# Performance work log

Measured on AMD Instinct MI355X. Metric: run time of the kernel, lower is better.

## Reference

```python
import jax, jax.numpy as jnp
import numpy as np

EMBED_DIM = 768
NUM_HEADS = 12
HEAD_DIM = EMBED_DIM // NUM_HEADS  # 64
NUM_LEVELS = 2
Q_INDEX = (0, 6, 12)  # head-axis split per level
K_INDEX = (0, 6, 12)
V_INDEX = (0, 6, 12)


def setup_inputs() -> dict:
    key = jax.random.key(0)
    ks = jax.random.split(key, 12)
    std = 0.02
    d = {
        'inp0': jax.random.normal(ks[0], (8, 2048, 768), jnp.float32),
        'inp1': jax.random.normal(ks[1], (8, 1024, 1536), jnp.float32),
        'attn_mask': jax.random.normal(ks[2], (8, HEAD_DIM), jnp.float32),
        'Wq0': jax.random.normal(ks[3], (768, 768), jnp.float32) * std,
        'bq0': jnp.zeros((768,), jnp.float32),
        'Wk0': jax.random.normal(ks[4], (768, 768), jnp.float32) * std,
        'bk0': jnp.zeros((768,), jnp.float32),
        'Wv0': jax.random.normal(ks[5], (768, 768), jnp.float32) * std,
        'bv0': jnp.zeros((768,), jnp.float32),
        'Wq1': jax.random.normal(ks[6], (1536, 768), jnp.float32) * std,
        'bq1': jnp.zeros((768,), jnp.float32),
        'Wk1': jax.random.normal(ks[7], (1536, 768), jnp.float32) * std,
        'bk1': jnp.zeros((768,), jnp.float32),
        'Wv1': jax.random.normal(ks[8], (1536, 768), jnp.float32) * std,
        'bv1': jnp.zeros((768,), jnp.float32),
        'Wo': jax.random.normal(ks[9], (2 * 768, 768), jnp.float32) * std,
        'bo': jnp.zeros((768,), jnp.float32),
    }
    return d


def _split_heads(x):
    b, n, _ = x.shape
    return x.reshape(b, n, NUM_HEADS, HEAD_DIM).transpose(0, 2, 1, 3)  # b h n d


def _level_attention(level, inp, Wq, bq, Wk, bk, Wv, bv, attn_mask):
    q = _split_heads(inp @ Wq + bq)[:, Q_INDEX[level]:Q_INDEX[level + 1]]
    k = _split_heads(inp @ Wk + bk)[:, K_INDEX[level]:K_INDEX[level + 1]]
    v = _split_heads(inp @ Wv + bv)[:, V_INDEX[level]:V_INDEX[level + 1]]
    q = q * (HEAD_DIM ** -0.5)
    q = q + attn_mask[:, None, None, :]  # broadcast mask over heads & positions
    scores = jnp.einsum('bhnd,bhmd->bhnm', q, k)
    attn = jax.nn.softmax(scores, axis=-1)
    return jnp.einsum('bhnm,bhmd->bhnd', attn, v)  # b h n d


def reference(inp0, inp1, attn_mask, Wq0, bq0, Wk0, bk0, Wv0, bv0,
              Wq1, bq1, Wk1, bk1, Wv1, bv1, Wo, bo):
    levels = [
        (inp0, Wq0, bq0, Wk0, bk0, Wv0, bv0),
        (inp1, Wq1, bq1, Wk1, bk1, Wv1, bv1),
    ]
    outputs = [_level_attention(l, *args, attn_mask) for l, args in enumerate(levels)]
    n_max = max(o.shape[2] for o in outputs)
    merged, masks = [], []
    for o in outputs:
        b, h, n, dd = o.shape
        x = o.transpose(0, 2, 1, 3).reshape(b, n, h * dd)  # b n (h d)
        x = jnp.pad(x, ((0, 0), (0, n_max - n), (0, EMBED_DIM - h * dd)))
        merged.append(x)
        masks.append(jnp.pad(jnp.ones((n,), jnp.float32), (0, n_max - n)))
    x = jnp.concatenate(merged, axis=-1)  # [b, n_max, NUM_LEVELS*EMBED_DIM]
    output_mask = jnp.stack(masks)  # [NUM_LEVELS, n_max]
    output = x @ Wo + bo
    return (output, output_mask)
```

## Files before the change

### kernel.cpp

```cpp
#include <hip/hip_runtime.h>
#include <cmath>

typedef __bf16 bf16x8 __attribute__((ext_vector_type(8)));
typedef float floatx4 __attribute__((ext_vector_type(4)));

typedef __attribute__((address_space(1))) const void* as1_cvp;
typedef __attribute__((address_space(3))) void* as3_vp;

__device__ __forceinline__ void stage16(const void* g, void* l) {
    __builtin_amdgcn_global_load_lds((as1_cvp)g, (as3_vp)l, 16, 0, 0);
}

__global__ void prep_all(
    const float* __restrict__ inp0, const float* __restrict__ inp1,
    const float* __restrict__ Wq0, const float* __restrict__ Wk0, const float* __restrict__ Wv0,
    const float* __restrict__ Wq1, const float* __restrict__ Wk1, const float* __restrict__ Wv1,
    const float* __restrict__ Wo,
    __bf16* __restrict__ Ab0, __bf16* __restrict__ Ab1,
    __bf16* __restrict__ WT0, __bf16* __restrict__ WT1, __bf16* __restrict__ WoT)
{
    __shared__ __bf16 tile[64][72];
    const int bx = blockIdx.x;
    const int tid = threadIdx.x;

    if (bx < 12288) {
        const float* in  = (bx < 6144) ? inp0 : inp1;
        __bf16*      out = (bx < 6144) ? Ab0  : Ab1;
        int t = (bx < 6144 ? bx : bx - 6144) * 256 + tid;
        floatx4 f0 = *(const floatx4*)&in[(size_t)t * 8];
        floatx4 f1 = *(const floatx4*)&in[(size_t)t * 8 + 4];
        bf16x8 o;
#pragma unroll
        for (int j = 0; j < 4; j++) { o[j] = (__bf16)f0[j]; o[4 + j] = (__bf16)f1[j]; }
        *(bf16x8*)&out[(size_t)t * 8] = o;
        return;
    }

    int lane = tid & 63, tr = tid >> 6;

    if (bx < 12936) {
        int seg1 = (bx >= 12504);
        int idx = seg1 ? bx - 12504 : bx - 12288;
        int nkb = seg1 ? 24 : 12;
        int Kd  = seg1 ? 1536 : 768;
        int off = seg1 ? 384 : 0;
        int k0 = (idx % nkb) * 64, c0 = (idx / nkb) * 64;
        int proj = c0 / 384;
        const float* src = seg1 ? ((proj == 0) ? Wq1 : (proj == 1) ? Wk1 : Wv1)
                                : ((proj == 0) ? Wq0 : (proj == 1) ? Wk0 : Wv0);
        __bf16* WT = seg1 ? WT1 : WT0;
        int col = off + (c0 % 384) + lane;
#pragma unroll
        for (int i = 0; i < 16; i++) {
            int r = i * 4 + tr;
            tile[lane][r] = (__bf16)src[(size_t)(k0 + r) * 768 + col];
        }
        __syncthreads();
#pragma unroll
        for (int i = 0; i < 16; i++) {
            int cl = i * 4 + tr;
            WT[(size_t)(c0 + cl) * Kd + k0 + lane] = tile[cl][lane];
        }
        return;
    }

    {
        int idx = bx - 12936;
        int k0 = (idx % 12) * 64, c0 = (idx / 12) * 64;
        int col = c0 + lane;
#pragma unroll
        for (int i = 0; i < 16; i++) {
            int k = k0 + i * 4 + tr;
            int srow = k + (k >= 384 ? 384 : 0);
            tile[lane][i * 4 + tr] = (__bf16)Wo[(size_t)srow * 768 + col];
        }
        __syncthreads();
#pragma unroll
        for (int i = 0; i < 16; i++) {
            int cl = i * 4 + tr;
            WoT[(size_t)(c0 + cl) * 768 + k0 + lane] = tile[cl][lane];
        }
        return;
    }
}

__global__ __launch_bounds__(256, 2) void qkv_all(
    const __bf16* __restrict__ Ab0, const __bf16* __restrict__ Ab1,
    const __bf16* __restrict__ WT0, const __bf16* __restrict__ WT1,
    const float* __restrict__ bq0, const float* __restrict__ bk0, const float* __restrict__ bv0,
    const float* __restrict__ bq1, const float* __restrict__ bk1, const float* __restrict__ bv1,
    const float* __restrict__ mask,
    __bf16* __restrict__ Q0, __bf16* __restrict__ K0, __bf16* __restrict__ V0T,
    __bf16* __restrict__ Q1, __bf16* __restrict__ K1, __bf16* __restrict__ V1T)
{
    __shared__ __bf16 As[128 * 64];
    __shared__ __bf16 Bs[128 * 64];
    const int bx = blockIdx.x;
    const int seg = (bx >= 1152);
    const int idx = seg ? bx - 1152 : bx;
    const int Kd  = seg ? 1536 : 768;
    const int Nl  = seg ? 1024 : 2048;
    const int nlsh = seg ? 10 : 11;
    const int off = seg ? 384 : 0;
    const __bf16* A  = seg ? Ab1 : Ab0;
    const __bf16* BT = seg ? WT1 : WT0;
    const float* bq = seg ? bq1 : bq0;
    const float* bk = seg ? bk1 : bk0;
    const float* bv = seg ? bv1 : bv0;
    __bf16* Qo  = seg ? Q1 : Q0;
    __bf16* Ko  = seg ? K1 : K0;
    __bf16* VTo = seg ? V1T : V0T;

    const int tid = threadIdx.x;
    const int lane = tid & 63;
    const int wave = tid >> 6;
    const int lr = lane & 15, lg = lane >> 4;
    const int col0 = (idx % 9) * 128, row0 = (idx / 9) * 128;
    const int qr = (wave >> 1) * 64, qc = (wave & 1) * 64;
    floatx4 acc[4][4] = {};

    for (int k0 = 0; k0 < Kd; k0 += 64) {
        const __bf16* ga = A + (size_t)(row0 + wave * 32 + (lane >> 3)) * Kd + k0 + (lane & 7) * 8;
        const __bf16* gb = BT + (size_t)(col0 + wave * 32 + (lane >> 3)) * Kd + k0 + (lane & 7) * 8;
#pragma unroll
        for (int i = 0; i < 4; i++) {
            stage16(ga + (size_t)i * 8 * Kd, &As[(wave * 32 + i * 8) * 64]);
            stage16(gb + (size_t)i * 8 * Kd, &Bs[(wave * 32 + i * 8) * 64]);
        }
        __syncthreads();
#pragma unroll
        for (int ch = 0; ch < 2; ch++) {
            bf16x8 af[4], bfr[4];
#pragma unroll
            for (int mt = 0; mt < 4; mt++)
                af[mt] = *(const bf16x8*)&As[(qr + mt * 16 + lr) * 64 + ch * 32 + lg * 8];
#pragma unroll
            for (int nt = 0; nt < 4; nt++)
                bfr[nt] = *(const bf16x8*)&Bs[(qc + nt * 16 + lr) * 64 + ch * 32 + lg * 8];
#pragma unroll
            for (int mt = 0; mt < 4; mt++)
#pragma unroll
                for (int nt = 0; nt < 4; nt++)
                    acc[mt][nt] = __builtin_amdgcn_mfma_f32_16x16x32_bf16(af[mt], bfr[nt], acc[mt][nt], 0, 0, 0);
        }
        __syncthreads();
    }

    const float S_Q = 0.125f * 1.44269504088896f;
    const float S_M = 1.44269504088896f;
#pragma unroll
    for (int nt = 0; nt < 4; nt++) {
        int C = col0 + qc + nt * 16 + lr;
        int proj = C / 384;
        int rem = C - proj * 384;
        int h = rem >> 6, d = C & 63;
        float bias = (proj == 0) ? bq[off + rem]
                   : (proj == 1) ? bk[off + rem]
                                 : bv[off + rem];
#pragma unroll
        for (int mt = 0; mt < 4; mt++) {
#pragma unroll
            for (int r = 0; r < 4; r++) {
                int R = row0 + qr + mt * 16 + lg * 4 + r;
                int b = R >> nlsh;
                int n = R & (Nl - 1);
                size_t hb = (size_t)(b * 6 + h);
                float v = acc[mt][nt][r] + bias;
                if (proj == 0) {
                    v = fmaf(v, S_Q, S_M * mask[(b << 6) + d]);
                    Qo[(hb * Nl + n) * 64 + d] = (__bf16)v;
                } else if (proj == 1) {
                    Ko[(hb * Nl + n) * 64 + d] = (__bf16)v;
                } else {
                    VTo[(hb * 64 + d) * (size_t)Nl + n] = (__bf16)v;
                }
            }
        }
    }
}

__global__ __launch_bounds__(256, 4) void attn_all(
    const __bf16* __restrict__ Q0, const __bf16* __restrict__ K0, const __bf16* __restrict__ V0T,
    const __bf16* __restrict__ Q1, const __bf16* __restrict__ K1, const __bf16* __restrict__ V1T,
    __bf16* __restrict__ X, float* __restrict__ om)
{
    __shared__ __bf16 Ks[64 * 72];
    __shared__ __bf16 Vs[64 * 72];
    __shared__ __bf16 Ps[4][32 * 72];
    const int bx = blockIdx.x;
    const int tid = threadIdx.x;

    if (bx >= 1152) {
        int t = (bx - 1152) * 256 + tid;
        int r = t / 48;
        int c = (t - r * 48) * 8;
        int b = r >> 10, n = 1024 + (r & 1023);
        floatx4 z = {0.f, 0.f, 0.f, 0.f};
        *(floatx4*)&X[(size_t)(b * 2048 + n) * 768 + 384 + c] = z;
        if (t < 4096)
            om[t] = (t < 2048) ? 1.0f : (((t - 2048) < 1024) ? 1.0f : 0.0f);
        return;
    }

    const int seg = (bx >= 768);
    const int idx = seg ? bx - 768 : bx;
    const int Nl = seg ? 1024 : 2048;
    const int qb = seg ? (idx & 7) : (idx & 15);
    const int rest = seg ? (idx >> 3) : (idx >> 4);
    const int h = rest % 6, b = rest / 6;
    const int xoff = seg ? 384 : 0;
    const __bf16* Q  = seg ? Q1 : Q0;
    const __bf16* K  = seg ? K1 : K0;
    const __bf16* VT = seg ? V1T : V0T;

    const int wave = tid >> 6, lane = tid & 63;
    const int lr = lane & 15, lg = lane >> 4;
    const size_t head = (size_t)(b * 6 + h) * Nl * 64;
    const int q0 = qb * 128 + wave * 16;

    bf16x8 qf[2][2];
#pragma unroll
    for (int s = 0; s < 2; s++)
#pragma unroll
        for (int ch = 0; ch < 2; ch++)
            qf[s][ch] = *(const bf16x8*)&Q[head + (size_t)(q0 + s * 64 + lr) * 64 + ch * 32 + lg * 8];

    bf16x8 onesv;
#pragma unroll
    for (int j = 0; j < 8; j++) onesv[j] = (__bf16)1.0f;

    const int rr = tid >> 2, cc = (tid & 3) * 16;
    const __bf16* Kg = K + head;
    const __bf16* Vg = VT + head;

    bf16x8 kr0, kr1, vr0, vr1;
    {
        size_t kb = (size_t)rr * 64 + cc;
        kr0 = *(const bf16x8*)&Kg[kb];
        kr1 = *(const bf16x8*)&Kg[kb + 8];
        size_t vb = (size_t)rr * Nl + cc;
        vr0 = *(const bf16x8*)&Vg[vb];
        vr1 = *(const bf16x8*)&Vg[vb + 8];
    }

    floatx4 o_acc[2][4] = {};
    floatx4 l_acc[2] = {};

    for (int n0 = 0; n0 < Nl; n0 += 64) {
        __syncthreads();
        *(bf16x8*)&Ks[rr * 72 + cc]     = kr0;
        *(bf16x8*)&Ks[rr * 72 + cc + 8] = kr1;
        *(bf16x8*)&Vs[rr * 72 + cc]     = vr0;
        *(bf16x8*)&Vs[rr * 72 + cc + 8] = vr1;
        __syncthreads();

        if (n0 + 64 < Nl) {
            size_t kb = (size_t)(n0 + 64 + rr) * 64 + cc;
            kr0 = *(const bf16x8*)&Kg[kb];
            kr1 = *(const bf16x8*)&Kg[kb + 8];
            size_t vb = (size_t)rr * Nl + n0 + 64 + cc;
            vr0 = *(const bf16x8*)&Vg[vb];
            vr1 = *(const bf16x8*)&Vg[vb + 8];
        }

        floatx4 sv[2][4] = {};
#pragma unroll
        for (int ch = 0; ch < 2; ch++) {
#pragma unroll
            for (int nt = 0; nt < 4; nt++) {
                bf16x8 kb8 = *(const bf16x8*)&Ks[(nt * 16 + lr) * 72 + ch * 32 + lg * 8];
                sv[0][nt] = __builtin_amdgcn_mfma_f32_16x16x32_bf16(qf[0][ch], kb8, sv[0][nt], 0, 0, 0);
                sv[1][nt] = __builtin_amdgcn_mfma_f32_16x16x32_bf16(qf[1][ch], kb8, sv[1][nt], 0, 0, 0);
            }
        }

#pragma unroll
        for (int s = 0; s < 2; s++)
#pragma unroll
            for (int nt = 0; nt < 4; nt++)
#pragma unroll
                for (int r = 0; r < 4; r++) {
                    float p = __builtin_amdgcn_exp2f(sv[s][nt][r]);
                    Ps[wave][(s * 16 + lg * 4 + r) * 72 + nt * 16 + lr] = (__bf16)p;
                }
        asm volatile("s_waitcnt lgkmcnt(0)" ::: "memory");

#pragma unroll
        for (int ch = 0; ch < 2; ch++) {
            bf16x8 pa0 = *(const bf16x8*)&Ps[wave][lr * 72 + ch * 32 + lg * 8];
            bf16x8 pa1 = *(const bf16x8*)&Ps[wave][(16 + lr) * 72 + ch * 32 + lg * 8];
#pragma unroll
            for (int dt = 0; dt < 4; dt++) {
                bf16x8 vb8 = *(const bf16x8*)&Vs[(dt * 16 + lr) * 72 + ch * 32 + lg * 8];
                o_acc[0][dt] = __builtin_amdgcn_mfma_f32_16x16x32_bf16(pa0, vb8, o_acc[0][dt], 0, 0, 0);
                o_acc[1][dt] = __builtin_amdgcn_mfma_f32_16x16x32_bf16(pa1, vb8, o_acc[1][dt], 0, 0, 0);
            }
            l_acc[0] = __builtin_amdgcn_mfma_f32_16x16x32_bf16(pa0, onesv, l_acc[0], 0, 0, 0);
            l_acc[1] = __builtin_amdgcn_mfma_f32_16x16x32_bf16(pa1, onesv, l_acc[1], 0, 0, 0);
        }
    }

#pragma unroll
    for (int s = 0; s < 2; s++)
#pragma unroll
        for (int dt = 0; dt < 4; dt++)
#pragma unroll
            for (int r = 0; r < 4; r++) {
                int n = q0 + s * 64 + lg * 4 + r;
                float o = o_acc[s][dt][r] / l_acc[s][r];
                X[(size_t)(b * 2048 + n) * 768 + xoff + h * 64 + dt * 16 + lr] = (__bf16)o;
            }
}

__global__ __launch_bounds__(256, 2) void out_gemm(
    const __bf16* __restrict__ A, const __bf16* __restrict__ BT,
    const float* __restrict__ bo, float* __restrict__ out)
{
    __shared__ __bf16 As[128 * 64];
    __shared__ __bf16 Bs[128 * 64];
    const int tid = threadIdx.x;
    const int lane = tid & 63;
    const int wave = tid >> 6;
    const int lr = lane & 15, lg = lane >> 4;
    const int col0 = blockIdx.x * 128, row0 = blockIdx.y * 128;
    const int qr = (wave >> 1) * 64, qc = (wave & 1) * 64;
    const int Kd = 768;
    floatx4 acc[4][4] = {};

    for (int k0 = 0; k0 < Kd; k0 += 64) {
        const __bf16* ga = A + (size_t)(row0 + wave * 32 + (lane >> 3)) * Kd + k0 + (lane & 7) * 8;
        const __bf16* gb = BT + (size_t)(col0 + wave * 32 + (lane >> 3)) * Kd + k0 + (lane & 7) * 8;
#pragma unroll
        for (int i = 0; i < 4; i++) {
            stage16(ga + (size_t)i * 8 * Kd, &As[(wave * 32 + i * 8) * 64]);
            stage16(gb + (size_t)i * 8 * Kd, &Bs[(wave * 32 + i * 8) * 64]);
        }
        __syncthreads();
#pragma unroll
        for (int ch = 0; ch < 2; ch++) {
            bf16x8 af[4], bfr[4];
#pragma unroll
            for (int mt = 0; mt < 4; mt++)
                af[mt] = *(const bf16x8*)&As[(qr + mt * 16 + lr) * 64 + ch * 32 + lg * 8];
#pragma unroll
            for (int nt = 0; nt < 4; nt++)
                bfr[nt] = *(const bf16x8*)&Bs[(qc + nt * 16 + lr) * 64 + ch * 32 + lg * 8];
#pragma unroll
            for (int mt = 0; mt < 4; mt++)
#pragma unroll
                for (int nt = 0; nt < 4; nt++)
                    acc[mt][nt] = __builtin_amdgcn_mfma_f32_16x16x32_bf16(af[mt], bfr[nt], acc[mt][nt], 0, 0, 0);
        }
        __syncthreads();
    }

#pragma unroll
    for (int nt = 0; nt < 4; nt++) {
        int C = col0 + qc + nt * 16 + lr;
        float bias = bo[C];
#pragma unroll
        for (int mt = 0; mt < 4; mt++) {
#pragma unroll
            for (int r = 0; r < 4; r++) {
                int R = row0 + qr + mt * 16 + lg * 4 + r;
                out[(size_t)R * 768 + C] = acc[mt][nt][r] + bias;
            }
        }
    }
}

extern "C" void kernel_launch(void* const* d_in, const int* in_sizes, int n_in,
                              void* d_out, int out_size, void* d_ws, size_t ws_size,
                              hipStream_t stream)
{
    const float* inp0  = (const float*)d_in[0];
    const float* inp1  = (const float*)d_in[1];
    const float* amask = (const float*)d_in[2];
    const float* Wq0 = (const float*)d_in[3];
    const float* bq0 = (const float*)d_in[4];
    const float* Wk0 = (const float*)d_in[5];
    const float* bk0 = (const float*)d_in[6];
    const float* Wv0 = (const float*)d_in[7];
    const float* bv0 = (const float*)d_in[8];
    const float* Wq1 = (const float*)d_in[9];
    const float* bq1 = (const float*)d_in[10];
    const float* Wk1 = (const float*)d_in[11];
    const float* bk1 = (const float*)d_in[12];
    const float* Wv1 = (const float*)d_in[13];
    const float* bv1 = (const float*)d_in[14];
    const float* Wo  = (const float*)d_in[15];
    const float* bo  = (const float*)d_in[16];

    char* ws = (char*)d_ws;
    __bf16* WT0 = (__bf16*)(ws + 0);
    __bf16* WT1 = (__bf16*)(ws + 1769472);
    __bf16* WoT = (__bf16*)(ws + 5308416);
    __bf16* Ab0 = (__bf16*)(ws + 6488064);
    __bf16* X   = Ab0;
    __bf16* Ab1 = (__bf16*)(ws + 31653888);
    __bf16* Q0  = (__bf16*)(ws + 56819712);
    __bf16* K0  = (__bf16*)(ws + 69402624);
    __bf16* V0T = (__bf16*)(ws + 81985536);
    __bf16* Q1  = (__bf16*)(ws + 94568448);
    __bf16* K1  = (__bf16*)(ws + 100859904);
    __bf16* V1T = (__bf16*)(ws + 107151360);
    float* outp = (float*)d_out;

    hipLaunchKernelGGL(prep_all, dim3(13080), dim3(256), 0, stream,
                       inp0, inp1, Wq0, Wk0, Wv0, Wq1, Wk1, Wv1, Wo,
                       Ab0, Ab1, WT0, WT1, WoT);
    hipLaunchKernelGGL(qkv_all, dim3(1728), dim3(256), 0, stream,
                       Ab0, Ab1, WT0, WT1,
                       bq0, bk0, bv0, bq1, bk1, bv1, amask,
                       Q0, K0, V0T, Q1, K1, V1T);
    hipLaunchKernelGGL(attn_all, dim3(2688), dim3(256), 0, stream,
                       Q0, K0, V0T, Q1, K1, V1T, X, outp + 12582912);
    hipLaunchKernelGGL(out_gemm, dim3(6, 128), dim3(256), 0, stream,
                       X, WoT, bo, outp);
}
```

Measured before the change: 437.3 us.

## Swizzle GEMM LDS tiles, remap blocks across XCDs, prioritize attention MFMA

Both GEMMs now load global 16-byte chunks with an XOR swizzle and read the LDS fragments with the matching XOR. This is meant to remove LDS bank conflicts on the fragment reads. Block indices in qkv, attention and output GEMM are remapped so that consecutive hardware block IDs, which are spread round-robin over the 8 XCDs, map to contiguous tiles. That should improve L2 locality per XCD. The attention loop also raises wave priority around its MFMA sections with s_setprio, and the output GEMM launch becomes a flat 1D grid.

```diff
diff --git a/kernel.cpp b/kernel.cpp
--- a/kernel.cpp
+++ b/kernel.cpp
@@ -95,7 +95,10 @@
 {
     __shared__ __bf16 As[128 * 64];
     __shared__ __bf16 Bs[128 * 64];
-    const int bx = blockIdx.x;
+    const int p = blockIdx.x;
+    int bx;
+    if (p < 1152) bx = (p & 7) * 144 + (p >> 3);
+    else { int q = p - 1152; bx = 1152 + (q & 7) * 72 + (q >> 3); }
     const int seg = (bx >= 1152);
     const int idx = seg ? bx - 1152 : bx;
     const int Kd  = seg ? 1536 : 768;
@@ -119,9 +122,11 @@
     const int qr = (wave >> 1) * 64, qc = (wave & 1) * 64;
     floatx4 acc[4][4] = {};
 
+    const int schunk = ((lane & 7) ^ (lane >> 3)) * 8;
+
     for (int k0 = 0; k0 < Kd; k0 += 64) {
-        const __bf16* ga = A + (size_t)(row0 + wave * 32 + (lane >> 3)) * Kd + k0 + (lane & 7) * 8;
-        const __bf16* gb = BT + (size_t)(col0 + wave * 32 + (lane >> 3)) * Kd + k0 + (lane & 7) * 8;
+        const __bf16* ga = A + (size_t)(row0 + wave * 32 + (lane >> 3)) * Kd + k0 + schunk;
+        const __bf16* gb = BT + (size_t)(col0 + wave * 32 + (lane >> 3)) * Kd + k0 + schunk;
 #pragma unroll
         for (int i = 0; i < 4; i++) {
             stage16(ga + (size_t)i * 8 * Kd, &As[(wave * 32 + i * 8) * 64]);
@@ -133,10 +138,12 @@
             bf16x8 af[4], bfr[4];
 #pragma unroll
             for (int mt = 0; mt < 4; mt++)
-                af[mt] = *(const bf16x8*)&As[(qr + mt * 16 + lr) * 64 + ch * 32 + lg * 8];
+                af[mt] = *(const bf16x8*)&As[(qr + mt * 16 + lr) * 64
+                                            + (((ch * 4 + lg) ^ (lr & 7)) * 8)];
 #pragma unroll
             for (int nt = 0; nt < 4; nt++)
-                bfr[nt] = *(const bf16x8*)&Bs[(qc + nt * 16 + lr) * 64 + ch * 32 + lg * 8];
+                bfr[nt] = *(const bf16x8*)&Bs[(qc + nt * 16 + lr) * 64
+                                             + (((ch * 4 + lg) ^ (lr & 7)) * 8)];
 #pragma unroll
             for (int mt = 0; mt < 4; mt++)
 #pragma unroll
@@ -187,7 +194,11 @@
     __shared__ __bf16 Ks[64 * 72];
     __shared__ __bf16 Vs[64 * 72];
     __shared__ __bf16 Ps[4][32 * 72];
-    const int bx = blockIdx.x;
+    const int p = blockIdx.x;
+    int bx;
+    if (p < 768) bx = (p & 7) * 96 + (p >> 3);
+    else if (p < 1152) { int q = p - 768; bx = 768 + (q & 7) * 48 + (q >> 3); }
+    else bx = p;
     const int tid = threadIdx.x;
 
     if (bx >= 1152) {
@@ -264,6 +275,7 @@
         }
 
         floatx4 sv[2][4] = {};
+        __builtin_amdgcn_s_setprio(1);
 #pragma unroll
         for (int ch = 0; ch < 2; ch++) {
 #pragma unroll
@@ -273,6 +285,7 @@
                 sv[1][nt] = __builtin_amdgcn_mfma_f32_16x16x32_bf16(qf[1][ch], kb8, sv[1][nt], 0, 0, 0);
             }
         }
+        __builtin_amdgcn_s_setprio(0);
 
 #pragma unroll
         for (int s = 0; s < 2; s++)
@@ -280,11 +293,12 @@
             for (int nt = 0; nt < 4; nt++)
 #pragma unroll
                 for (int r = 0; r < 4; r++) {
-                    float p = __builtin_amdgcn_exp2f(sv[s][nt][r]);
-                    Ps[wave][(s * 16 + lg * 4 + r) * 72 + nt * 16 + lr] = (__bf16)p;
+                    float p2 = __builtin_amdgcn_exp2f(sv[s][nt][r]);
+                    Ps[wave][(s * 16 + lg * 4 + r) * 72 + nt * 16 + lr] = (__bf16)p2;
                 }
         asm volatile("s_waitcnt lgkmcnt(0)" ::: "memory");
 
+        __builtin_amdgcn_s_setprio(1);
 #pragma unroll
         for (int ch = 0; ch < 2; ch++) {
             bf16x8 pa0 = *(const bf16x8*)&Ps[wave][lr * 72 + ch * 32 + lg * 8];
@@ -298,6 +312,7 @@
             l_acc[0] = __builtin_amdgcn_mfma_f32_16x16x32_bf16(pa0, onesv, l_acc[0], 0, 0, 0);
             l_acc[1] = __builtin_amdgcn_mfma_f32_16x16x32_bf16(pa1, onesv, l_acc[1], 0, 0, 0);
         }
+        __builtin_amdgcn_s_setprio(0);
     }
 
 #pragma unroll
@@ -322,14 +337,18 @@
     const int lane = tid & 63;
     const int wave = tid >> 6;
     const int lr = lane & 15, lg = lane >> 4;
-    const int col0 = blockIdx.x * 128, row0 = blockIdx.y * 128;
+    const int p = blockIdx.x;
+    const int bx = (p & 7) * 96 + (p >> 3);
+    const int col0 = (bx % 6) * 128, row0 = (bx / 6) * 128;
     const int qr = (wave >> 1) * 64, qc = (wave & 1) * 64;
     const int Kd = 768;
     floatx4 acc[4][4] = {};
 
+    const int schunk = ((lane & 7) ^ (lane >> 3)) * 8;
+
     for (int k0 = 0; k0 < Kd; k0 += 64) {
-        const __bf16* ga = A + (size_t)(row0 + wave * 32 + (lane >> 3)) * Kd + k0 + (lane & 7) * 8;
-        const __bf16* gb = BT + (size_t)(col0 + wave * 32 + (lane >> 3)) * Kd + k0 + (lane & 7) * 8;
+        const __bf16* ga = A + (size_t)(row0 + wave * 32 + (lane >> 3)) * Kd + k0 + schunk;
+        const __bf16* gb = BT + (size_t)(col0 + wave * 32 + (lane >> 3)) * Kd + k0 + schunk;
 #pragma unroll
         for (int i = 0; i < 4; i++) {
             stage16(ga + (size_t)i * 8 * Kd, &As[(wave * 32 + i * 8) * 64]);
@@ -341,10 +360,12 @@
             bf16x8 af[4], bfr[4];
 #pragma unroll
             for (int mt = 0; mt < 4; mt++)
-                af[mt] = *(const bf16x8*)&As[(qr + mt * 16 + lr) * 64 + ch * 32 + lg * 8];
+                af[mt] = *(const bf16x8*)&As[(qr + mt * 16 + lr) * 64
+                                            + (((ch * 4 + lg) ^ (lr & 7)) * 8)];
 #pragma unroll
             for (int nt = 0; nt < 4; nt++)
-                bfr[nt] = *(const bf16x8*)&Bs[(qc + nt * 16 + lr) * 64 + ch * 32 + lg * 8];
+                bfr[nt] = *(const bf16x8*)&Bs[(qc + nt * 16 + lr) * 64
+                                             + (((ch * 4 + lg) ^ (lr & 7)) * 8)];
 #pragma unroll
             for (int mt = 0; mt < 4; mt++)
 #pragma unroll
@@ -415,6 +436,6 @@
                        Q0, K0, V0T, Q1, K1, V1T);
     hipLaunchKernelGGL(attn_all, dim3(2688), dim3(256), 0, stream,
                        Q0, K0, V0T, Q1, K1, V1T, X, outp + 12582912);
-    hipLaunchKernelGGL(out_gemm, dim3(6, 128), dim3(256), 0, stream,
+    hipLaunchKernelGGL(out_gemm, dim3(768), dim3(256), 0, stream,
                        X, WoT, bo, outp);
 }
```

Result: faster. 408.7 us (-6.5%).
